# Performance work log

Measured on AMD Instinct MI355X. Metric: run time of the kernel, lower is better.

The kernel has to match this reference:

```python
import jax, jax.numpy as jnp
import numpy as np

DIM_IN = 1024
DIM_Q = 1024
DIM_K = 1024
DIM_V = 1024
HEADS = 16

def setup_inputs() -> dict:
    key = jax.random.key(0)
    ks = jax.random.split(key, 5)
    s = 1.0 / np.sqrt(DIM_IN)
    return {
        "x": jax.random.normal(ks[0], (2, 2048, DIM_IN), dtype=jnp.float32),
        "Wq": jax.random.uniform(ks[1], (DIM_IN, DIM_Q), jnp.float32, -s, s),
        "Wk": jax.random.uniform(ks[2], (DIM_IN, DIM_K), jnp.float32, -s, s),
        "Wv": jax.random.uniform(ks[3], (DIM_IN, DIM_V), jnp.float32, -s, s),
        "Wo": jax.random.uniform(ks[4], (DIM_V, DIM_V), jnp.float32, -1.0/np.sqrt(DIM_V), 1.0/np.sqrt(DIM_V)),
    }

def reference(x, Wq, Wk, Wv, Wo):
    B, S, _ = x.shape
    H = HEADS
    q = (x @ Wq).reshape(B, S, H, DIM_Q // H).transpose(0, 2, 1, 3)  # [B,H,S,dq]
    k = (x @ Wk).reshape(B, S, H, DIM_K // H).transpose(0, 2, 1, 3)
    v = (x @ Wv).reshape(B, S, H, DIM_V // H).transpose(0, 2, 1, 3)
    scores = jnp.einsum("bhsd,bhtd->bhst", q, k)  # no pre-softmax scaling (as in source)
    # NOTE: source divides by sqrt(dim_q) AFTER softmax — replicated faithfully.
    attn = jax.nn.softmax(scores, axis=-1) / jnp.sqrt(jnp.float32(DIM_Q))
    out = jnp.einsum("bhst,bhtd->bhsd", attn, v)  # [B,H,S,dv]
    out = out.transpose(0, 2, 1, 3).reshape(B, S, DIM_V)
    return out @ Wo
```

## Files before the change

### kernel.cpp

```cpp
#include <hip/hip_runtime.h>
#include <hip/hip_bf16.h>


typedef __attribute__((ext_vector_type(8))) short bf16x8;
typedef __attribute__((ext_vector_type(4))) short short4v;
typedef __attribute__((ext_vector_type(4))) float f32x4;
typedef __attribute__((ext_vector_type(2))) unsigned int u32x2;

typedef const __attribute__((address_space(1))) void gvoid_t;
typedef __attribute__((address_space(3))) void svoid_t;
#define GLDS16(g, l) \
  __builtin_amdgcn_global_load_lds((gvoid_t*)(g), (svoid_t*)(l), 16, 0, 0)

#define MFMA16(a, b, c) __builtin_amdgcn_mfma_f32_16x16x32_bf16((a), (b), (c), 0, 0, 0)

#if defined(__has_builtin)
#if __has_builtin(__builtin_amdgcn_exp2f)
#define EXP2(x) __builtin_amdgcn_exp2f(x)
#else
#define EXP2(x) exp2f(x)
#endif
#else
#define EXP2(x) exp2f(x)
#endif

#define LOG2E 1.4426950408889634f
#define NSHIFT 17.312340490667561f

static __device__ __forceinline__ short f2bf(float f) {
  __hip_bfloat16 h = __float2bfloat16(f);
  short s;
  __builtin_memcpy(&s, &h, 2);
  return s;
}

static __device__ __forceinline__ unsigned pack2bf(float lo, float hi) {
  float2 t; t.x = lo; t.y = hi;
  __hip_bfloat162 h2 = __float22bfloat162_rn(t);
  unsigned u;
  __builtin_memcpy(&u, &h2, 4);
  return u;
}

__global__ __launch_bounds__(256) void prep(const float* __restrict__ x,
                                            const float* __restrict__ Wq,
                                            const float* __restrict__ Wk,
                                            const float* __restrict__ Wv,
                                            const float* __restrict__ Wo,
                                            short* __restrict__ xb,
                                            short* __restrict__ wqkvt,
                                            short* __restrict__ wot) {
  __shared__ float tile[64][65];
  int bid = blockIdx.x;
  int tid = threadIdx.x;
  if (bid < 2048) {
    int i = bid * 256 + tid;
    const float4* p = (const float4*)(x + (size_t)i * 8);
    float4 a = p[0], b = p[1];
    bf16x8 o;
    o[0] = f2bf(a.x); o[1] = f2bf(a.y); o[2] = f2bf(a.z); o[3] = f2bf(a.w);
    o[4] = f2bf(b.x); o[5] = f2bf(b.y); o[6] = f2bf(b.z); o[7] = f2bf(b.w);
    *(bf16x8*)(xb + (size_t)i * 8) = o;
    return;
  }
  bid -= 2048;
  int mat = bid >> 8;
  int t = bid & 255;
  int tn = (t & 15) * 64;
  int tk = (t >> 4) * 64;
  const float* src = (mat == 0) ? Wq : (mat == 1) ? Wk : (mat == 2) ? Wv : Wo;
  short* dst = (mat < 3) ? (wqkvt + (size_t)mat * 1024 * 1024) : wot;

  int c4 = (tid & 15) * 4;
#pragma unroll
  for (int it = 0; it < 4; ++it) {
    int r = (tid >> 4) + it * 16;
    float4 v = *(const float4*)(src + (size_t)(tk + r) * 1024 + tn + c4);
    tile[r][c4 + 0] = v.x; tile[r][c4 + 1] = v.y;
    tile[r][c4 + 2] = v.z; tile[r][c4 + 3] = v.w;
  }
  __syncthreads();
  int n = tid >> 2;
  int kc = (tid & 3) * 16;
  bf16x8 o0, o1;
#pragma unroll
  for (int j = 0; j < 8; ++j) {
    o0[j] = f2bf(tile[kc + j][n]);
    o1[j] = f2bf(tile[kc + 8 + j][n]);
  }
  *(bf16x8*)(dst + (size_t)(tn + n) * 1024 + tk + kc) = o0;
  *(bf16x8*)(dst + (size_t)(tn + n) * 1024 + tk + kc + 8) = o1;
}

__global__ __launch_bounds__(512, 2) void gemm_qkv(const short* __restrict__ A,
                                                   const short* __restrict__ Bt,
                                                   short* __restrict__ qk,
                                                   short* __restrict__ vt) {
  constexpr int K = 1024;
  __shared__ short As[2][256 * 64];
  __shared__ short Bs[2][256 * 64];
  const int tid = threadIdx.x;
  const int lane = tid & 63;
  const int w = tid >> 6;
  const int lr = lane & 15, lg = lane >> 4;
  const int m0 = blockIdx.y * 256, n0 = blockIdx.x * 256;
  const int wm = (w >> 2) * 128, wn = (w & 3) * 64;

  auto stage = [&](int kt, int bb) {
#pragma unroll
    for (int it = 0; it < 4; ++it) {
      int id = it * 512 + tid;
      int row = id >> 3, c = id & 7;
      int sc = c ^ (row & 7);
      GLDS16(A + (size_t)(m0 + row) * K + kt + sc * 8, &As[bb][0] + id * 8);
      GLDS16(Bt + (size_t)(n0 + row) * K + kt + sc * 8, &Bs[bb][0] + id * 8);
    }
  };

  f32x4 acc[8][4] = {};

  stage(0, 0);
  __syncthreads();

  int cur = 0;
  for (int kt = 0; kt < K; kt += 64) {
    if (kt + 64 < K) stage(kt + 64, cur ^ 1);
    const short* Ab = &As[cur][0];
    const short* Bb = &Bs[cur][0];
#pragma unroll
    for (int kk2 = 0; kk2 < 2; ++kk2) {
      bf16x8 bfr[4];
#pragma unroll
      for (int ni = 0; ni < 4; ++ni) {
        int row = wn + ni * 16 + lr;
        int cw = kk2 * 4 + lg;
        bfr[ni] = *(const bf16x8*)(Bb + row * 64 + ((cw ^ (row & 7)) * 8));
      }
      __builtin_amdgcn_s_setprio(1);
#pragma unroll
      for (int mi = 0; mi < 8; ++mi) {
        int row = wm + mi * 16 + lr;
        int cw = kk2 * 4 + lg;
        bf16x8 af = *(const bf16x8*)(Ab + row * 64 + ((cw ^ (row & 7)) * 8));
#pragma unroll
        for (int ni = 0; ni < 4; ++ni)
          acc[mi][ni] = MFMA16(af, bfr[ni], acc[mi][ni]);
      }
      __builtin_amdgcn_s_setprio(0);
    }
    __syncthreads();
    cur ^= 1;
  }

  if (n0 < 2048) {
#pragma unroll
    for (int mi = 0; mi < 8; ++mi) {
#pragma unroll
      for (int ni = 0; ni < 4; ++ni) {
        int m = m0 + wm + mi * 16 + lg * 4;
        int n = n0 + wn + ni * 16 + lr;
#pragma unroll
        for (int r = 0; r < 4; ++r)
          qk[(size_t)(m + r) * 2048 + n] = f2bf(acc[mi][ni][r]);
      }
    }
  } else {
#pragma unroll
    for (int mi = 0; mi < 8; ++mi) {
#pragma unroll
      for (int ni = 0; ni < 4; ++ni) {
        int m = m0 + wm + mi * 16 + lg * 4;
        int nv = n0 + wn + ni * 16 + lr - 2048;
        int vtrow = ((m >> 11) * 16 + (nv >> 6)) * 64 + (nv & 63);
        int scol = m & 2047;
        short4v pv;
#pragma unroll
        for (int r = 0; r < 4; ++r) pv[r] = f2bf(acc[mi][ni][r]);
        *(short4v*)(vt + (size_t)vtrow * 2048 + scol) = pv;
      }
    }
  }
}

__global__ __launch_bounds__(256) void gemm_out(const short* __restrict__ A,
                                                const short* __restrict__ Bt,
                                                float* __restrict__ C) {
  constexpr int K = 1024, N = 1024;
  __shared__ short As[2][128 * 64];
  __shared__ short Bs[2][64 * 64];
  const int tid = threadIdx.x;
  const int lane = tid & 63;
  const int w = tid >> 6;
  const int lr = lane & 15, lg = lane >> 4;
  const int m0 = blockIdx.y * 128, n0 = blockIdx.x * 64;
  const int wm = (w >> 1) * 64, wn = (w & 1) * 32;

  auto stage = [&](int kt, int bb) {
#pragma unroll
    for (int it = 0; it < 4; ++it) {
      int id = it * 256 + tid;
      int row = id >> 3, c = id & 7;
      int sc = c ^ (row & 7);
      GLDS16(A + (size_t)(m0 + row) * K + kt + sc * 8, &As[bb][0] + id * 8);
    }
#pragma unroll
    for (int it = 0; it < 2; ++it) {
      int id = it * 256 + tid;
      int row = id >> 3, c = id & 7;
      int sc = c ^ (row & 7);
      GLDS16(Bt + (size_t)(n0 + row) * K + kt + sc * 8, &Bs[bb][0] + id * 8);
    }
  };

  f32x4 acc[4][2] = {};

  stage(0, 0);
  __syncthreads();

  int cur = 0;
  for (int kt = 0; kt < K; kt += 64) {
    if (kt + 64 < K) stage(kt + 64, cur ^ 1);
    const short* Ab = &As[cur][0];
    const short* Bb = &Bs[cur][0];
#pragma unroll
    for (int kk2 = 0; kk2 < 2; ++kk2) {
      bf16x8 bfr[2];
#pragma unroll
      for (int ni = 0; ni < 2; ++ni) {
        int row = wn + ni * 16 + lr;
        int cw = kk2 * 4 + lg;
        bfr[ni] = *(const bf16x8*)(Bb + row * 64 + ((cw ^ (row & 7)) * 8));
      }
      __builtin_amdgcn_s_setprio(1);
#pragma unroll
      for (int mi = 0; mi < 4; ++mi) {
        int row = wm + mi * 16 + lr;
        int cw = kk2 * 4 + lg;
        bf16x8 af = *(const bf16x8*)(Ab + row * 64 + ((cw ^ (row & 7)) * 8));
#pragma unroll
        for (int ni = 0; ni < 2; ++ni)
          acc[mi][ni] = MFMA16(af, bfr[ni], acc[mi][ni]);
      }
      __builtin_amdgcn_s_setprio(0);
    }
    __syncthreads();
    cur ^= 1;
  }

#pragma unroll
  for (int mi = 0; mi < 4; ++mi) {
#pragma unroll
    for (int ni = 0; ni < 2; ++ni) {
      int m = m0 + wm + mi * 16 + lg * 4;
      int n = n0 + wn + ni * 16 + lr;
#pragma unroll
      for (int r = 0; r < 4; ++r) C[(size_t)(m + r) * N + n] = acc[mi][ni][r];
    }
  }
}

__device__ __forceinline__ void softmax_nm(const f32x4 s[4], float& lsum,
                                           u32x2 pk[4]) {
  float ls = 0.f;
#pragma unroll
  for (int kc = 0; kc < 4; ++kc) {
    float p0 = EXP2(fmaf(s[kc][0], LOG2E, -NSHIFT));
    float p1 = EXP2(fmaf(s[kc][1], LOG2E, -NSHIFT));
    float p2 = EXP2(fmaf(s[kc][2], LOG2E, -NSHIFT));
    float p3 = EXP2(fmaf(s[kc][3], LOG2E, -NSHIFT));
    ls += (p0 + p1) + (p2 + p3);
    pk[kc][0] = pack2bf(p0, p1);
    pk[kc][1] = pack2bf(p2, p3);
  }
  lsum += ls;
}

__global__ __launch_bounds__(256) void attn_fwd(const short* __restrict__ qk,
                                                const short* __restrict__ vt,
                                                short* __restrict__ outb) {
  constexpr int S = 2048, LDQ = 2048;
  const int fid = blockIdx.x;
  const int xcd = fid & 7, j = fid >> 3;
  const int qt = j & 15;
  const int pair = xcd * 4 + (j >> 4);
  const int h = pair & 15, b = pair >> 4;

  const int tid = threadIdx.x, lane = tid & 63, w = tid >> 6;
  const int lr = lane & 15, lg = lane >> 4;
  const int s7 = lr & 7;
  const int qb = qt * 128 + w * 32;

  __shared__ short Ks[2][64][64];
  __shared__ short Vs[2][64][64];
  __shared__ short Ps[4][32][64];

  const short* base = qk + (size_t)b * S * LDQ + h * 64;
  const short* vbase = vt + (size_t)(b * 16 + h) * 64 * 2048;

  bf16x8 qA0 = *(const bf16x8*)(base + (size_t)(qb + lr) * LDQ + lg * 8);
  bf16x8 qA1 = *(const bf16x8*)(base + (size_t)(qb + lr) * LDQ + 32 + lg * 8);
  bf16x8 qB0 = *(const bf16x8*)(base + (size_t)(qb + 16 + lr) * LDQ + lg * 8);
  bf16x8 qB1 = *(const bf16x8*)(base + (size_t)(qb + 16 + lr) * LDQ + 32 + lg * 8);

  auto stage = [&](int kt, int bb) {
#pragma unroll
    for (int it = 0; it < 2; ++it) {
      int id = it * 256 + tid;
      int row = id >> 3, c = id & 7;
      int sc = c ^ (row & 7);
      GLDS16(base + 1024 + (size_t)(kt + row) * LDQ + sc * 8,
             &Ks[bb][0][0] + id * 8);
      GLDS16(vbase + (size_t)row * 2048 + kt + sc * 8,
             &Vs[bb][0][0] + id * 8);
    }
  };

  f32x4 oA[4] = {}, oB[4] = {};
  float lA = 0.f, lB = 0.f;

  stage(0, 0);
  __syncthreads();

  int cur = 0;
  for (int kt = 0; kt < S; kt += 64) {
    if (kt + 64 < S) stage(kt + 64, cur ^ 1);

    const short* Kb = &Ks[cur][0][0];
    const short* Vb = &Vs[cur][0][0];
    short* Pw = &Ps[w][0][0];

    f32x4 sA[4], sB[4];
    __builtin_amdgcn_s_setprio(1);
#pragma unroll
    for (int kc = 0; kc < 4; ++kc) {
      int krow = kc * 16 + lr;
      bf16x8 kf0 = *(const bf16x8*)(Kb + krow * 64 + ((lg ^ s7) * 8));
      bf16x8 kf1 = *(const bf16x8*)(Kb + krow * 64 + (((4 + lg) ^ s7) * 8));
      f32x4 s = {};
      s = MFMA16(kf0, qA0, s);
      s = MFMA16(kf1, qA1, s);
      sA[kc] = s;
      f32x4 t = {};
      t = MFMA16(kf0, qB0, t);
      t = MFMA16(kf1, qB1, t);
      sB[kc] = t;
    }
    __builtin_amdgcn_s_setprio(0);

    u32x2 pkA[4], pkB[4];
    softmax_nm(sA, lA, pkA);
    softmax_nm(sB, lB, pkB);

#pragma unroll
    for (int kc = 0; kc < 4; ++kc) {
      int pc = ((2 * kc + (lg >> 1)) ^ s7) * 8 + (lg & 1) * 4;
      *(u32x2*)(Pw + lr * 64 + pc) = pkA[kc];
      *(u32x2*)(Pw + (16 + lr) * 64 + pc) = pkB[kc];
    }

    __builtin_amdgcn_s_setprio(1);
#pragma unroll
    for (int kk = 0; kk < 2; ++kk) {
      int pch = ((4 * kk + lg) ^ s7) * 8;
      bf16x8 pA = *(const bf16x8*)(Pw + lr * 64 + pch);
      bf16x8 pB = *(const bf16x8*)(Pw + (16 + lr) * 64 + pch);
#pragma unroll
      for (int nc = 0; nc < 4; ++nc) {
        bf16x8 vf = *(const bf16x8*)(Vb + (nc * 16 + lr) * 64 + pch);
        oA[nc] = MFMA16(pA, vf, oA[nc]);
        oB[nc] = MFMA16(pB, vf, oB[nc]);
      }
    }
    __builtin_amdgcn_s_setprio(0);
    __syncthreads();
    cur ^= 1;
  }

  float ltA = lA + __shfl_xor(lA, 16);
  ltA += __shfl_xor(ltA, 32);
  float ltB = lB + __shfl_xor(lB, 16);
  ltB += __shfl_xor(ltB, 32);
#pragma unroll
  for (int r = 0; r < 4; ++r) {
    float dA = 1.0f / (__shfl(ltA, 4 * lg + r) * 32.0f);
    float dB = 1.0f / (__shfl(ltB, 4 * lg + r) * 32.0f);
#pragma unroll
    for (int nc = 0; nc < 4; ++nc) {
      int col = h * 64 + nc * 16 + lr;
      outb[(size_t)(b * S + qb + 4 * lg + r) * 1024 + col] = f2bf(oA[nc][r] * dA);
      outb[(size_t)(b * S + qb + 16 + 4 * lg + r) * 1024 + col] =
          f2bf(oB[nc][r] * dB);
    }
  }
}

extern "C" void kernel_launch(void* const* d_in, const int* in_sizes, int n_in,
                              void* d_out, int out_size, void* d_ws,
                              size_t ws_size, hipStream_t stream) {
  (void)in_sizes; (void)n_in; (void)out_size; (void)ws_size;
  const float* x = (const float*)d_in[0];
  const float* Wq = (const float*)d_in[1];
  const float* Wk = (const float*)d_in[2];
  const float* Wv = (const float*)d_in[3];
  const float* Wo = (const float*)d_in[4];

  char* p = (char*)d_ws;
  short* xb = (short*)p;      p += (size_t)4096 * 1024 * 2;
  short* wqkvt = (short*)p;   p += (size_t)3072 * 1024 * 2;
  short* wot = (short*)p;     p += (size_t)1024 * 1024 * 2;
  short* qk = (short*)p;      p += (size_t)4096 * 2048 * 2;
  short* vt = (short*)p;      p += (size_t)4096 * 1024 * 2;
  short* attno = (short*)p;   p += (size_t)4096 * 1024 * 2;

  prep<<<3072, 256, 0, stream>>>(x, Wq, Wk, Wv, Wo, xb, wqkvt, wot);
  gemm_qkv<<<dim3(12, 16), 512, 0, stream>>>(xb, wqkvt, qk, vt);
  attn_fwd<<<512, 256, 0, stream>>>(qk, vt, attno);
  gemm_out<<<dim3(16, 32), 256, 0, stream>>>(attno, wot, (float*)d_out);
}
```

Baseline: 122.6 us.

## Shrink QKV GEMM tiles, fold log2e into Q, double attention waves per block

```diff
diff --git a/kernel.cpp b/kernel.cpp
--- a/kernel.cpp
+++ b/kernel.cpp
@@ -92,32 +92,38 @@
   *(bf16x8*)(dst + (size_t)(tn + n) * 1024 + tk + kc + 8) = o1;
 }
 
-__global__ __launch_bounds__(512, 2) void gemm_qkv(const short* __restrict__ A,
+__global__ __launch_bounds__(512, 4) void gemm_qkv(const short* __restrict__ A,
                                                    const short* __restrict__ Bt,
                                                    short* __restrict__ qk,
                                                    short* __restrict__ vt) {
   constexpr int K = 1024;
-  __shared__ short As[2][256 * 64];
-  __shared__ short Bs[2][256 * 64];
+  __shared__ short As[2][128 * 64];
+  __shared__ short Bs[2][192 * 64];
   const int tid = threadIdx.x;
   const int lane = tid & 63;
   const int w = tid >> 6;
   const int lr = lane & 15, lg = lane >> 4;
-  const int m0 = blockIdx.y * 256, n0 = blockIdx.x * 256;
-  const int wm = (w >> 2) * 128, wn = (w & 3) * 64;
+  const int m0 = blockIdx.y * 128, n0 = blockIdx.x * 192;
+  const int wm = (w >> 2) * 64, wn = (w & 3) * 48;
 
   auto stage = [&](int kt, int bb) {
 #pragma unroll
-    for (int it = 0; it < 4; ++it) {
+    for (int it = 0; it < 2; ++it) {
       int id = it * 512 + tid;
       int row = id >> 3, c = id & 7;
       int sc = c ^ (row & 7);
       GLDS16(A + (size_t)(m0 + row) * K + kt + sc * 8, &As[bb][0] + id * 8);
+    }
+#pragma unroll
+    for (int it = 0; it < 3; ++it) {
+      int id = it * 512 + tid;
+      int row = id >> 3, c = id & 7;
+      int sc = c ^ (row & 7);
       GLDS16(Bt + (size_t)(n0 + row) * K + kt + sc * 8, &Bs[bb][0] + id * 8);
     }
   };
 
-  f32x4 acc[8][4] = {};
+  f32x4 acc[4][3] = {};
 
   stage(0, 0);
   __syncthreads();
@@ -129,21 +135,20 @@
     const short* Bb = &Bs[cur][0];
 #pragma unroll
     for (int kk2 = 0; kk2 < 2; ++kk2) {
-      bf16x8 bfr[4];
-#pragma unroll
-      for (int ni = 0; ni < 4; ++ni) {
+      int cw = kk2 * 4 + lg;
+      bf16x8 bfr[3];
+#pragma unroll
+      for (int ni = 0; ni < 3; ++ni) {
         int row = wn + ni * 16 + lr;
-        int cw = kk2 * 4 + lg;
         bfr[ni] = *(const bf16x8*)(Bb + row * 64 + ((cw ^ (row & 7)) * 8));
       }
       __builtin_amdgcn_s_setprio(1);
 #pragma unroll
-      for (int mi = 0; mi < 8; ++mi) {
+      for (int mi = 0; mi < 4; ++mi) {
         int row = wm + mi * 16 + lr;
-        int cw = kk2 * 4 + lg;
         bf16x8 af = *(const bf16x8*)(Ab + row * 64 + ((cw ^ (row & 7)) * 8));
 #pragma unroll
-        for (int ni = 0; ni < 4; ++ni)
+        for (int ni = 0; ni < 3; ++ni)
           acc[mi][ni] = MFMA16(af, bfr[ni], acc[mi][ni]);
       }
       __builtin_amdgcn_s_setprio(0);
@@ -152,25 +157,19 @@
     cur ^= 1;
   }
 
-  if (n0 < 2048) {
-#pragma unroll
-    for (int mi = 0; mi < 8; ++mi) {
-#pragma unroll
-      for (int ni = 0; ni < 4; ++ni) {
-        int m = m0 + wm + mi * 16 + lg * 4;
-        int n = n0 + wn + ni * 16 + lr;
+#pragma unroll
+  for (int mi = 0; mi < 4; ++mi) {
+#pragma unroll
+    for (int ni = 0; ni < 3; ++ni) {
+      int m = m0 + wm + mi * 16 + lg * 4;
+      int n = n0 + wn + ni * 16 + lr;
+      if (n < 2048) {
+        float sc = (n < 1024) ? LOG2E : 1.0f;
 #pragma unroll
         for (int r = 0; r < 4; ++r)
-          qk[(size_t)(m + r) * 2048 + n] = f2bf(acc[mi][ni][r]);
-      }
-    }
-  } else {
-#pragma unroll
-    for (int mi = 0; mi < 8; ++mi) {
-#pragma unroll
-      for (int ni = 0; ni < 4; ++ni) {
-        int m = m0 + wm + mi * 16 + lg * 4;
-        int nv = n0 + wn + ni * 16 + lr - 2048;
+          qk[(size_t)(m + r) * 2048 + n] = f2bf(acc[mi][ni][r] * sc);
+      } else {
+        int nv = n - 2048;
         int vtrow = ((m >> 11) * 16 + (nv >> 6)) * 64 + (nv & 63);
         int scol = m & 2047;
         short4v pv;
@@ -224,18 +223,17 @@
     const short* Bb = &Bs[cur][0];
 #pragma unroll
     for (int kk2 = 0; kk2 < 2; ++kk2) {
+      int cw = kk2 * 4 + lg;
       bf16x8 bfr[2];
 #pragma unroll
       for (int ni = 0; ni < 2; ++ni) {
         int row = wn + ni * 16 + lr;
-        int cw = kk2 * 4 + lg;
         bfr[ni] = *(const bf16x8*)(Bb + row * 64 + ((cw ^ (row & 7)) * 8));
       }
       __builtin_amdgcn_s_setprio(1);
 #pragma unroll
       for (int mi = 0; mi < 4; ++mi) {
         int row = wm + mi * 16 + lr;
-        int cw = kk2 * 4 + lg;
         bf16x8 af = *(const bf16x8*)(Ab + row * 64 + ((cw ^ (row & 7)) * 8));
 #pragma unroll
         for (int ni = 0; ni < 2; ++ni)
@@ -264,10 +262,10 @@
   float ls = 0.f;
 #pragma unroll
   for (int kc = 0; kc < 4; ++kc) {
-    float p0 = EXP2(fmaf(s[kc][0], LOG2E, -NSHIFT));
-    float p1 = EXP2(fmaf(s[kc][1], LOG2E, -NSHIFT));
-    float p2 = EXP2(fmaf(s[kc][2], LOG2E, -NSHIFT));
-    float p3 = EXP2(fmaf(s[kc][3], LOG2E, -NSHIFT));
+    float p0 = EXP2(s[kc][0]);
+    float p1 = EXP2(s[kc][1]);
+    float p2 = EXP2(s[kc][2]);
+    float p3 = EXP2(s[kc][3]);
     ls += (p0 + p1) + (p2 + p3);
     pk[kc][0] = pack2bf(p0, p1);
     pk[kc][1] = pack2bf(p2, p3);
@@ -275,9 +273,9 @@
   lsum += ls;
 }
 
-__global__ __launch_bounds__(256) void attn_fwd(const short* __restrict__ qk,
-                                                const short* __restrict__ vt,
-                                                short* __restrict__ outb) {
+__global__ __launch_bounds__(512, 4) void attn_fwd(const short* __restrict__ qk,
+                                                   const short* __restrict__ vt,
+                                                   short* __restrict__ outb) {
   constexpr int S = 2048, LDQ = 2048;
   const int fid = blockIdx.x;
   const int xcd = fid & 7, j = fid >> 3;
@@ -288,35 +286,30 @@
   const int tid = threadIdx.x, lane = tid & 63, w = tid >> 6;
   const int lr = lane & 15, lg = lane >> 4;
   const int s7 = lr & 7;
-  const int qb = qt * 128 + w * 32;
+  const int qb = qt * 128 + w * 16;
 
   __shared__ short Ks[2][64][64];
   __shared__ short Vs[2][64][64];
-  __shared__ short Ps[4][32][64];
+  __shared__ short Ps[8][16][64];
 
   const short* base = qk + (size_t)b * S * LDQ + h * 64;
   const short* vbase = vt + (size_t)(b * 16 + h) * 64 * 2048;
 
   bf16x8 qA0 = *(const bf16x8*)(base + (size_t)(qb + lr) * LDQ + lg * 8);
   bf16x8 qA1 = *(const bf16x8*)(base + (size_t)(qb + lr) * LDQ + 32 + lg * 8);
-  bf16x8 qB0 = *(const bf16x8*)(base + (size_t)(qb + 16 + lr) * LDQ + lg * 8);
-  bf16x8 qB1 = *(const bf16x8*)(base + (size_t)(qb + 16 + lr) * LDQ + 32 + lg * 8);
 
   auto stage = [&](int kt, int bb) {
-#pragma unroll
-    for (int it = 0; it < 2; ++it) {
-      int id = it * 256 + tid;
-      int row = id >> 3, c = id & 7;
-      int sc = c ^ (row & 7);
-      GLDS16(base + 1024 + (size_t)(kt + row) * LDQ + sc * 8,
-             &Ks[bb][0][0] + id * 8);
-      GLDS16(vbase + (size_t)row * 2048 + kt + sc * 8,
-             &Vs[bb][0][0] + id * 8);
-    }
+    int id = tid;
+    int row = id >> 3, c = id & 7;
+    int sc = c ^ (row & 7);
+    GLDS16(base + 1024 + (size_t)(kt + row) * LDQ + sc * 8,
+           &Ks[bb][0][0] + id * 8);
+    GLDS16(vbase + (size_t)row * 2048 + kt + sc * 8,
+           &Vs[bb][0][0] + id * 8);
   };
 
-  f32x4 oA[4] = {}, oB[4] = {};
-  float lA = 0.f, lB = 0.f;
+  f32x4 oA[4] = {};
+  float lA = 0.f;
 
   stage(0, 0);
   __syncthreads();
@@ -329,33 +322,27 @@
     const short* Vb = &Vs[cur][0][0];
     short* Pw = &Ps[w][0][0];
 
-    f32x4 sA[4], sB[4];
+    f32x4 sA[4];
     __builtin_amdgcn_s_setprio(1);
 #pragma unroll
     for (int kc = 0; kc < 4; ++kc) {
       int krow = kc * 16 + lr;
       bf16x8 kf0 = *(const bf16x8*)(Kb + krow * 64 + ((lg ^ s7) * 8));
       bf16x8 kf1 = *(const bf16x8*)(Kb + krow * 64 + (((4 + lg) ^ s7) * 8));
-      f32x4 s = {};
+      f32x4 s = {-NSHIFT, -NSHIFT, -NSHIFT, -NSHIFT};
       s = MFMA16(kf0, qA0, s);
       s = MFMA16(kf1, qA1, s);
       sA[kc] = s;
-      f32x4 t = {};
-      t = MFMA16(kf0, qB0, t);
-      t = MFMA16(kf1, qB1, t);
-      sB[kc] = t;
     }
     __builtin_amdgcn_s_setprio(0);
 
-    u32x2 pkA[4], pkB[4];
+    u32x2 pkA[4];
     softmax_nm(sA, lA, pkA);
-    softmax_nm(sB, lB, pkB);
 
 #pragma unroll
     for (int kc = 0; kc < 4; ++kc) {
       int pc = ((2 * kc + (lg >> 1)) ^ s7) * 8 + (lg & 1) * 4;
       *(u32x2*)(Pw + lr * 64 + pc) = pkA[kc];
-      *(u32x2*)(Pw + (16 + lr) * 64 + pc) = pkB[kc];
     }
 
     __builtin_amdgcn_s_setprio(1);
@@ -363,12 +350,10 @@
     for (int kk = 0; kk < 2; ++kk) {
       int pch = ((4 * kk + lg) ^ s7) * 8;
       bf16x8 pA = *(const bf16x8*)(Pw + lr * 64 + pch);
-      bf16x8 pB = *(const bf16x8*)(Pw + (16 + lr) * 64 + pch);
 #pragma unroll
       for (int nc = 0; nc < 4; ++nc) {
         bf16x8 vf = *(const bf16x8*)(Vb + (nc * 16 + lr) * 64 + pch);
         oA[nc] = MFMA16(pA, vf, oA[nc]);
-        oB[nc] = MFMA16(pB, vf, oB[nc]);
       }
     }
     __builtin_amdgcn_s_setprio(0);
@@ -378,18 +363,13 @@
 
   float ltA = lA + __shfl_xor(lA, 16);
   ltA += __shfl_xor(ltA, 32);
-  float ltB = lB + __shfl_xor(lB, 16);
-  ltB += __shfl_xor(ltB, 32);
 #pragma unroll
   for (int r = 0; r < 4; ++r) {
     float dA = 1.0f / (__shfl(ltA, 4 * lg + r) * 32.0f);
-    float dB = 1.0f / (__shfl(ltB, 4 * lg + r) * 32.0f);
 #pragma unroll
     for (int nc = 0; nc < 4; ++nc) {
       int col = h * 64 + nc * 16 + lr;
       outb[(size_t)(b * S + qb + 4 * lg + r) * 1024 + col] = f2bf(oA[nc][r] * dA);
-      outb[(size_t)(b * S + qb + 16 + 4 * lg + r) * 1024 + col] =
-          f2bf(oB[nc][r] * dB);
     }
   }
 }
@@ -413,7 +393,7 @@
   short* attno = (short*)p;   p += (size_t)4096 * 1024 * 2;
 
   prep<<<3072, 256, 0, stream>>>(x, Wq, Wk, Wv, Wo, xb, wqkvt, wot);
-  gemm_qkv<<<dim3(12, 16), 512, 0, stream>>>(xb, wqkvt, qk, vt);
-  attn_fwd<<<512, 256, 0, stream>>>(qk, vt, attno);
+  gemm_qkv<<<dim3(16, 32), 512, 0, stream>>>(xb, wqkvt, qk, vt);
+  attn_fwd<<<512, 512, 0, stream>>>(qk, vt, attno);
   gemm_out<<<dim3(16, 32), 256, 0, stream>>>(attno, wot, (float*)d_out);
 }
```

Measured after the change: 113.0 us. 1.09x faster.
